# Optimization experiments

Measured on AMD Instinct MI355X. Metric: run time of the kernel, lower is better.

## Reference

```python
import jax, jax.numpy as jnp
import numpy as np

H = 1024
VOCAB = 32000


def setup_inputs() -> dict:
    key = jax.random.key(0)
    ks = jax.random.split(key, 16)
    N, B, T = 32, 64, 400
    s = 1.0 / np.sqrt(H)
    inp = {
        "input_seq": jax.random.randint(ks[0], (N, B), 0, VOCAB),
        "last_hidden": jax.random.normal(ks[1], (1, B, H), jnp.float32),
        "encoder_outputs": jax.random.normal(ks[2], (T, B, H), jnp.float32),
        "encoderB_outputs": jax.random.normal(ks[3], (T, B, H), jnp.float32),
        # parameters
        "emb": jax.random.normal(ks[4], (VOCAB, H), jnp.float32),
        "W_ih": jax.random.uniform(ks[5], (3 * H, H), jnp.float32, -s, s),
        "W_hh": jax.random.uniform(ks[6], (3 * H, H), jnp.float32, -s, s),
        "b_ih": jax.random.uniform(ks[7], (3 * H,), jnp.float32, -s, s),
        "b_hh": jax.random.uniform(ks[8], (3 * H,), jnp.float32, -s, s),
        "attn_W": jax.random.uniform(ks[9], (H, 2 * H), jnp.float32, -s, s),
        "attn_b": jax.random.uniform(ks[10], (H,), jnp.float32, -s, s),
        "attn_v": jax.random.uniform(ks[11], (H,), jnp.float32, -s, s),
        "concat_W": jax.random.uniform(ks[12], (H, 3 * H), jnp.float32, -s, s),
        "concat_b": jax.random.uniform(ks[13], (H,), jnp.float32, -s, s),
        "out_W": jax.random.uniform(ks[14], (VOCAB, H), jnp.float32, -s, s),
        "out_b": jax.random.uniform(ks[15], (VOCAB,), jnp.float32, -s, s),
    }
    return inp


def _gru(x, h0, W_ih, W_hh, b_ih, b_hh):
    # x: (N,B,H), h0: (B,H). PyTorch GRU cell equations.
    def step(h, x_t):
        gi = x_t @ W_ih.T + b_ih          # (B,3H)
        gh = h @ W_hh.T + b_hh
        i_r, i_z, i_n = jnp.split(gi, 3, axis=-1)
        h_r, h_z, h_n = jnp.split(gh, 3, axis=-1)
        r = jax.nn.sigmoid(i_r + h_r)
        z = jax.nn.sigmoid(i_z + h_z)
        n = jnp.tanh(i_n + r * h_n)
        h_new = (1.0 - z) * n + z * h
        return h_new, h_new
    hN, outs = jax.lax.scan(step, h0, x)
    return outs, hN


def _attention(rnn_out, enc, attn_W, attn_b, v):
    # score(h, e) = (Linear([h; e]) ) . v  -- linear in both, so separable.
    W1, W2 = attn_W[:, :H], attn_W[:, H:]
    u1 = W1.T @ v                         # (H,)
    u2 = W2.T @ v
    bias = attn_b @ v                     # scalar
    a = rnn_out @ u1                      # (N,B)
    c = enc @ u2 + bias                   # (T,B)
    # energies (B,N,T), softmax over T (matches F.softmax on (-1, max_len))
    e = a.T[:, :, None] + c.T[:, None, :]
    w = jax.nn.softmax(e, axis=-1)        # (B,N,T)
    ctx = jnp.einsum('bnt,tbh->nbh', w, enc)  # bmm then transpose(0,1)
    return w, ctx


def reference(input_seq, last_hidden, encoder_outputs, encoderB_outputs,
              emb, W_ih, W_hh, b_ih, b_hh, attn_W, attn_b, attn_v,
              concat_W, concat_b, out_W, out_b):
    x = emb[input_seq]                                   # (N,B,H)
    rnn_out, hN = _gru(x, last_hidden[0], W_ih, W_hh, b_ih, b_hh)
    hidden = hN[None]                                    # (1,B,H)
    uw, u_ctx = _attention(rnn_out, encoder_outputs, attn_W, attn_b, attn_v)
    bw, b_ctx = _attention(rnn_out, encoderB_outputs, attn_W, attn_b, attn_v)
    cat = jnp.concatenate([rnn_out, u_ctx, b_ctx], axis=2)   # (N,B,3H)
    h = jnp.tanh(cat @ concat_W.T + concat_b)
    output = h @ out_W.T + out_b                          # (N,B,VOCAB)
    return output, hidden, uw, bw
```

## Files before the change

### kernel.cpp

```cpp
#include <hip/hip_runtime.h>
#include <cstdint>
#include <cstddef>

namespace {

constexpr int kH  = 1024;
constexpr int kB  = 64;
constexpr int kN  = 32;
constexpr int kT  = 400;
constexpr int kV  = 32000;
constexpr int kM  = kN * kB;
constexpr int k3H = 3 * kH;

typedef _Float16 f16;
typedef _Float16 f16x4 __attribute__((ext_vector_type(4)));
typedef _Float16 f16x8 __attribute__((ext_vector_type(8)));
typedef float    f32x4v __attribute__((ext_vector_type(4)));

__device__ __forceinline__ void gload_lds16(const void* g, void* l) {
  __builtin_amdgcn_global_load_lds((__attribute__((address_space(1))) void*)g,
                                   (__attribute__((address_space(3))) void*)l,
                                   16, 0, 0);
}

__device__ __forceinline__ uint32_t pack_f16x2(f16 lo, f16 hi) {
  union { f16 h[2]; uint32_t u; } c;
  c.h[0] = lo; c.h[1] = hi;
  return c.u;
}


__global__ void cvt_f16_kernel(const float* __restrict__ src, f16* __restrict__ dst, int n4) {
  int i = blockIdx.x * blockDim.x + threadIdx.x;
  const int stride = gridDim.x * blockDim.x;
  for (; i < n4; i += stride) {
    float4 v = reinterpret_cast<const float4*>(src)[i];
    f16x4 o = { (f16)v.x, (f16)v.y, (f16)v.z, (f16)v.w };
    reinterpret_cast<f16x4*>(dst)[i] = o;
  }
}

__global__ void gather_x_kernel(const int* __restrict__ seq, const float* __restrict__ emb,
                                f16* __restrict__ xh) {
  const int m = blockIdx.x;
  const int tok = seq[m];
  float4 v = reinterpret_cast<const float4*>(emb + (size_t)tok * kH)[threadIdx.x];
  f16x4 o = { (f16)v.x, (f16)v.y, (f16)v.z, (f16)v.w };
  reinterpret_cast<f16x4*>(xh + (size_t)m * kH)[threadIdx.x] = o;
}

__global__ void init_h_kernel(const float* __restrict__ lh, f16* __restrict__ hh0) {
  const int i = blockIdx.x * blockDim.x + threadIdx.x;
  float4 v = reinterpret_cast<const float4*>(lh)[i];
  f16x4 o = { (f16)v.x, (f16)v.y, (f16)v.z, (f16)v.w };
  reinterpret_cast<f16x4*>(hh0)[i] = o;
}

__global__ void attn_prep_kernel(const float* __restrict__ attn_W, const float* __restrict__ attn_b,
                                 const float* __restrict__ v, float* __restrict__ u2,
                                 float* __restrict__ biasS) {
  const int h = blockIdx.x;
  const int lane = threadIdx.x;
  float sum = 0.0f;
  if (h < kH) {
    for (int k = lane; k < kH; k += 64)
      sum += attn_W[(size_t)k * (2 * kH) + kH + h] * v[k];
  } else {
    for (int k = lane; k < kH; k += 64)
      sum += attn_b[k] * v[k];
  }
  #pragma unroll
  for (int o = 32; o > 0; o >>= 1) sum += __shfl_xor(sum, o);
  if (lane == 0) {
    if (h < kH) u2[h] = sum; else biasS[0] = sum;
  }
}


template <bool TANH, bool NT, typename OUT_T>
__global__ __launch_bounds__(256)
void gemm_bt_kernel(const f16* __restrict__ A, const f16* __restrict__ Bt,
                    const float* __restrict__ bias, OUT_T* __restrict__ C,
                    int M, int N, int K) {
  __shared__ __align__(16) f16 As[128 * 64];
  __shared__ __align__(16) f16 Bs[128 * 64];
  const int tid  = threadIdx.x;
  const int wave = tid >> 6;
  const int lane = tid & 63;
  const int m0 = blockIdx.x * 128;
  const int n0 = blockIdx.y * 128;
  const int wm = (wave >> 1) * 64;
  const int wn = (wave & 1) * 64;
  const int rsub = lane >> 3;
  const int coff = (lane & 7) * 8;
  f32x4v acc[4][4] = {};
  const int nk = K >> 6;
  for (int kc = 0; kc < nk; ++kc) {
    const f16* Ag = A + (size_t)m0 * K + kc * 64;
    const f16* Bg = Bt + (size_t)n0 * K + kc * 64;
    for (int c = wave; c < 16; c += 4) {
      const int row = c * 8 + rsub;
      gload_lds16(Ag + (size_t)row * K + coff, &As[c * 512]);
      gload_lds16(Bg + (size_t)row * K + coff, &Bs[c * 512]);
    }
    __syncthreads();
    #pragma unroll
    for (int kk = 0; kk < 2; ++kk) {
      const int ko = kk * 32 + (lane >> 4) * 8;
      f16x8 af[4], bfr[4];
      #pragma unroll
      for (int i = 0; i < 4; ++i) {
        af[i]  = *reinterpret_cast<const f16x8*>(&As[(wm + i * 16 + (lane & 15)) * 64 + ko]);
        bfr[i] = *reinterpret_cast<const f16x8*>(&Bs[(wn + i * 16 + (lane & 15)) * 64 + ko]);
      }
      #pragma unroll
      for (int mi = 0; mi < 4; ++mi)
        #pragma unroll
        for (int ni = 0; ni < 4; ++ni)
          acc[mi][ni] = __builtin_amdgcn_mfma_f32_16x16x32_f16(af[mi], bfr[ni], acc[mi][ni], 0, 0, 0);
    }
    __syncthreads();
  }
  const int rb = (lane >> 4) * 4;
  const int cb = lane & 15;
  #pragma unroll
  for (int mi = 0; mi < 4; ++mi) {
    #pragma unroll
    for (int ni = 0; ni < 4; ++ni) {
      const int col = n0 + wn + ni * 16 + cb;
      const float bv = bias[col];
      #pragma unroll
      for (int r = 0; r < 4; ++r) {
        const int row = m0 + wm + mi * 16 + rb + r;
        float v = acc[mi][ni][r] + bv;
        if (TANH) v = tanhf(v);
        if (NT) __builtin_nontemporal_store((OUT_T)v, &C[(size_t)row * N + col]);
        else C[(size_t)row * N + col] = (OUT_T)v;
      }
    }
  }
}


constexpr int kGruBlks = 64;
constexpr int kAttnBlks = 128;
constexpr int kCvtBlks = 320;
constexpr int kMegaBlks = kGruBlks + kAttnBlks + kCvtBlks;

__global__ __launch_bounds__(256, 1)
void mega_kernel(const f16* __restrict__ Whh, const float* __restrict__ bhh,
                 const float* __restrict__ gi, const float* __restrict__ lh,
                 f16* __restrict__ HHa, f16* __restrict__ HHb,
                 f16* __restrict__ cath, float* __restrict__ hiddenOut,
                 unsigned int* __restrict__ flags,
                 const float* __restrict__ enc0, const float* __restrict__ enc1,
                 const float* __restrict__ u2, const float* __restrict__ biasS,
                 float* __restrict__ uw, float* __restrict__ bw,
                 const float* __restrict__ oW, f16* __restrict__ oWh,
                 const float* __restrict__ cW, f16* __restrict__ cWh) {
  __shared__ union SM {
    float ghp[4][64][52];
    struct { float4 u2s[256]; float srow[kT]; float red[8]; } at;
  } sm;
  const int bid = blockIdx.x;
  const int tid = threadIdx.x;

  if (bid < kGruBlks) {
    const int wave = tid >> 6;
    const int lane = tid & 63;
    const int ln   = lane & 15;
    const int khi  = lane >> 4;
    const int j0   = bid * 16;
    const int kw   = wave * 256;
    const int fm   = tid >> 2;
    const int fc   = (tid & 3) * 4;
    const int myprod = wave * 16 + ln;

    f16x8 bfr[3][8];
    #pragma unroll
    for (int s = 0; s < 3; ++s)
      #pragma unroll
      for (int ks = 0; ks < 8; ++ks)
        bfr[s][ks] = *reinterpret_cast<const f16x8*>(
            &Whh[(size_t)(s * kH + j0 + ln) * kH + kw + ks * 32 + khi * 8]);

    float hreg[4], bR[4], bZ[4], bN[4];
    #pragma unroll
    for (int e = 0; e < 4; ++e) {
      const int j = j0 + fc + e;
      hreg[e] = lh[(size_t)fm * kH + j];
      bR[e] = bhh[j]; bZ[e] = bhh[kH + j]; bN[e] = bhh[2 * kH + j];
    }

    for (int step = 0; step < kN; ++step) {
      const f16* hh  = (step & 1) ? HHb : HHa;
      f16*       hho = (step & 1) ? HHa : HHb;

      float4 giL[3];
      {
        const size_t mm = (size_t)step * kB + fm;
        #pragma unroll
        for (int s = 0; s < 3; ++s)
          giL[s] = *reinterpret_cast<const float4*>(&gi[mm * k3H + s * kH + j0 + fc]);
      }

      if (step > 0) {
        while (true) {
          unsigned int f = __hip_atomic_load(&flags[myprod], __ATOMIC_RELAXED,
                                             __HIP_MEMORY_SCOPE_SYSTEM);
          if (__all(f >= (unsigned int)step)) break;
          __builtin_amdgcn_s_sleep(1);
        }
        __builtin_amdgcn_fence(__ATOMIC_ACQUIRE, "agent");
      }

      f16x8 af[8][4];
      #pragma unroll
      for (int ks = 0; ks < 8; ++ks)
        #pragma unroll
        for (int mi = 0; mi < 4; ++mi)
          af[ks][mi] = *reinterpret_cast<const f16x8*>(
              &hh[(size_t)(mi * 16 + ln) * kH + kw + ks * 32 + khi * 8]);

      f32x4v acc[4][3] = {};
      #pragma unroll
      for (int ks = 0; ks < 8; ++ks)
        #pragma unroll
        for (int mi = 0; mi < 4; ++mi)
          #pragma unroll
          for (int s = 0; s < 3; ++s)
            acc[mi][s] = __builtin_amdgcn_mfma_f32_16x16x32_f16(af[ks][mi], bfr[s][ks], acc[mi][s], 0, 0, 0);

      #pragma unroll
      for (int mi = 0; mi < 4; ++mi)
        #pragma unroll
        for (int s = 0; s < 3; ++s)
          #pragma unroll
          for (int r = 0; r < 4; ++r)
            sm.ghp[wave][mi * 16 + khi * 4 + r][s * 16 + ln] = acc[mi][s][r];
      __syncthreads();

      float4 gr4 = {0,0,0,0}, gz4 = {0,0,0,0}, gn4 = {0,0,0,0};
      #pragma unroll
      for (int w = 0; w < 4; ++w) {
        float4 a = *reinterpret_cast<const float4*>(&sm.ghp[w][fm][fc]);
        float4 b = *reinterpret_cast<const float4*>(&sm.ghp[w][fm][16 + fc]);
        float4 c = *reinterpret_cast<const float4*>(&sm.ghp[w][fm][32 + fc]);
        gr4.x += a.x; gr4.y += a.y; gr4.z += a.z; gr4.w += a.w;
        gz4.x += b.x; gz4.y += b.y; gz4.z += b.z; gz4.w += b.w;
        gn4.x += c.x; gn4.y += c.y; gn4.z += c.z; gn4.w += c.w;
      }
      float hv[4];
      const float* grp = &gr4.x; const float* gzp = &gz4.x; const float* gnp = &gn4.x;
      const float* gil0 = &giL[0].x; const float* gil1 = &giL[1].x; const float* gil2 = &giL[2].x;
      #pragma unroll
      for (int e = 0; e < 4; ++e) {
        const float r  = 1.0f / (1.0f + expf(-(gil0[e] + grp[e] + bR[e])));
        const float z  = 1.0f / (1.0f + expf(-(gil1[e] + gzp[e] + bZ[e])));
        const float nn = tanhf(gil2[e] + r * (gnp[e] + bN[e]));
        hv[e] = (1.0f - z) * nn + z * hreg[e];
        hreg[e] = hv[e];
      }
      const uint32_t p01 = pack_f16x2((f16)hv[0], (f16)hv[1]);
      const uint32_t p23 = pack_f16x2((f16)hv[2], (f16)hv[3]);
      const unsigned long long pk64 = (unsigned long long)p01 | ((unsigned long long)p23 << 32);
      __hip_atomic_store(reinterpret_cast<unsigned long long*>(&hho[(size_t)fm * kH + j0 + fc]),
                         pk64, __ATOMIC_RELAXED, __HIP_MEMORY_SCOPE_AGENT);
      __syncthreads();
      if (step < kN - 1 && tid == 0)
        __hip_atomic_store(&flags[bid], (unsigned int)(step + 1),
                           __ATOMIC_RELAXED, __HIP_MEMORY_SCOPE_SYSTEM);
      uint2 pku; pku.x = p01; pku.y = p23;
      *reinterpret_cast<uint2*>(&cath[((size_t)step * kB + fm) * k3H + j0 + fc]) = pku;
      if (step == kN - 1) {
        float4 hv4 = { hv[0], hv[1], hv[2], hv[3] };
        *reinterpret_cast<float4*>(&hiddenOut[(size_t)fm * kH + j0 + fc]) = hv4;
      }
    }
  } else if (bid < kGruBlks + kAttnBlks) {
    const int idx = bid - kGruBlks;
    const int e = idx >> 6, b = idx & 63;
    const float* enc = e ? enc1 : enc0;
    const int wave = tid >> 6, lane = tid & 63;

    sm.at.u2s[tid] = *reinterpret_cast<const float4*>(&u2[tid * 4]);
    __syncthreads();
    const float bias = biasS[0];

    for (int t = wave; t < kT; t += 4) {
      const float* row = enc + ((size_t)t * kB + b) * kH + lane * 16;
      float s = 0.0f;
      #pragma unroll
      for (int i = 0; i < 4; ++i) {
        float4 ev = reinterpret_cast<const float4*>(row)[i];
        float4 uv = sm.at.u2s[lane * 4 + i];
        s += ev.x * uv.x + ev.y * uv.y + ev.z * uv.z + ev.w * uv.w;
      }
      #pragma unroll
      for (int o = 32; o > 0; o >>= 1) s += __shfl_xor(s, o);
      if (lane == 0) sm.at.srow[t] = s + bias;
    }
    __syncthreads();

    float lmax = -1e30f;
    for (int t = tid; t < kT; t += 256) lmax = fmaxf(lmax, sm.at.srow[t]);
    #pragma unroll
    for (int o = 32; o > 0; o >>= 1) lmax = fmaxf(lmax, __shfl_xor(lmax, o));
    if (lane == 0) sm.at.red[wave] = lmax;
    __syncthreads();
    const float m = fmaxf(fmaxf(sm.at.red[0], sm.at.red[1]), fmaxf(sm.at.red[2], sm.at.red[3]));
    float lsum = 0.0f;
    for (int t = tid; t < kT; t += 256) {
      float ev = expf(sm.at.srow[t] - m);
      sm.at.srow[t] = ev;
      lsum += ev;
    }
    #pragma unroll
    for (int o = 32; o > 0; o >>= 1) lsum += __shfl_xor(lsum, o);
    if (lane == 0) sm.at.red[4 + wave] = lsum;
    __syncthreads();
    const float inv = 1.0f / (sm.at.red[4] + sm.at.red[5] + sm.at.red[6] + sm.at.red[7]);
    for (int t = tid; t < kT; t += 256) sm.at.srow[t] *= inv;
    __syncthreads();

    float* outp = (e ? bw : uw) + (size_t)b * kN * kT;
    for (int n = 0; n < kN; ++n)
      for (int t = tid; t < kT; t += 256)
        __builtin_nontemporal_store(sm.at.srow[t], &outp[n * kT + t]);

    const int j = tid * 4;
    float4 acc = {0,0,0,0};
    for (int t = 0; t < kT; ++t) {
      const float wt = sm.at.srow[t];
      const float4 ev = *reinterpret_cast<const float4*>(&enc[((size_t)t * kB + b) * kH + j]);
      acc.x += wt * ev.x; acc.y += wt * ev.y; acc.z += wt * ev.z; acc.w += wt * ev.w;
    }
    f16x4 cv = { (f16)acc.x, (f16)acc.y, (f16)acc.z, (f16)acc.w };
    #pragma unroll
    for (int n = 0; n < kN; ++n)
      *reinterpret_cast<f16x4*>(&cath[((size_t)(n * kB + b)) * k3H + kH + e * kH + j]) = cv;
  } else {
    constexpr int nOW = kV * kH / 4;
    constexpr int nCW = kH * k3H / 4;
    const int stride = kCvtBlks * 256;
    for (int i = (bid - kGruBlks - kAttnBlks) * 256 + tid; i < nOW + nCW; i += stride) {
      if (i < nOW) {
        float4 v = reinterpret_cast<const float4*>(oW)[i];
        f16x4 o = { (f16)v.x, (f16)v.y, (f16)v.z, (f16)v.w };
        reinterpret_cast<f16x4*>(oWh)[i] = o;
      } else {
        const int k = i - nOW;
        float4 v = reinterpret_cast<const float4*>(cW)[k];
        f16x4 o = { (f16)v.x, (f16)v.y, (f16)v.z, (f16)v.w };
        reinterpret_cast<f16x4*>(cWh)[k] = o;
      }
    }
  }
}

}


extern "C" void kernel_launch(void* const* d_in, const int* in_sizes, int n_in,
                              void* d_out, int out_size, void* d_ws, size_t ws_size,
                              hipStream_t stream) {
  (void)in_sizes; (void)n_in; (void)out_size; (void)ws_size;
  const int*   seq    = (const int*)d_in[0];
  const float* lh     = (const float*)d_in[1];
  const float* enc0   = (const float*)d_in[2];
  const float* enc1   = (const float*)d_in[3];
  const float* emb    = (const float*)d_in[4];
  const float* W_ih   = (const float*)d_in[5];
  const float* W_hh   = (const float*)d_in[6];
  const float* b_ih   = (const float*)d_in[7];
  const float* b_hh   = (const float*)d_in[8];
  const float* attn_W = (const float*)d_in[9];
  const float* attn_b = (const float*)d_in[10];
  const float* attn_v = (const float*)d_in[11];
  const float* cW     = (const float*)d_in[12];
  const float* cb     = (const float*)d_in[13];
  const float* oW     = (const float*)d_in[14];
  const float* ob     = (const float*)d_in[15];
  float* out = (float*)d_out;

  char* ws = (char*)d_ws;
  constexpr size_t oWih = 0;
  constexpr size_t oWhh = oWih + 6291456;
  constexpr size_t oCW  = oWhh + 6291456;
  constexpr size_t oOW  = oCW + 6291456;
  constexpr size_t oX   = oOW + 65536000;
  constexpr size_t oGI  = oX + 4194304;
  constexpr size_t oH0  = oGI + 25165824;
  constexpr size_t oH1  = oH0 + 262144;
  constexpr size_t oHH0 = oH1 + 262144;
  constexpr size_t oHH1 = oHH0 + 131072;
  constexpr size_t oCAT = oHH1 + 131072;
  constexpr size_t oH2  = oCAT + 12582912;
  constexpr size_t oU2  = oH2 + 4194304;
  constexpr size_t oBS  = oU2 + 4096;
  constexpr size_t oC   = oBS + 256;
  constexpr size_t oWSM = oC + 204800;
  constexpr size_t oCTR = oWSM + 204800;

  f16*   Wih_h = (f16*)(ws + oWih);
  f16*   Whh_h = (f16*)(ws + oWhh);
  f16*   cW_h  = (f16*)(ws + oCW);
  f16*   oW_h  = (f16*)(ws + oOW);
  f16*   X_h   = (f16*)(ws + oX);
  float* GI    = (float*)(ws + oGI);
  f16*   HH0   = (f16*)(ws + oHH0);
  f16*   HH1   = (f16*)(ws + oHH1);
  f16*   CAT   = (f16*)(ws + oCAT);
  f16*   H2    = (f16*)(ws + oH2);
  float* U2    = (float*)(ws + oU2);
  float* BS    = (float*)(ws + oBS);
  unsigned int* FLAGS = (unsigned int*)(ws + oCTR);

  constexpr size_t oHidden = (size_t)kM * kV;
  constexpr size_t oUW = oHidden + (size_t)kB * kH;
  constexpr size_t oBW = oUW + (size_t)kB * kN * kT;

  cvt_f16_kernel<<<1024, 256, 0, stream>>>(W_ih, Wih_h, k3H * kH / 4);
  cvt_f16_kernel<<<1024, 256, 0, stream>>>(W_hh, Whh_h, k3H * kH / 4);
  gather_x_kernel<<<kM, 256, 0, stream>>>(seq, emb, X_h);
  init_h_kernel<<<64, 256, 0, stream>>>(lh, HH0);
  attn_prep_kernel<<<1025, 64, 0, stream>>>(attn_W, attn_b, attn_v, U2, BS);
  hipMemsetAsync(FLAGS, 0, 64 * sizeof(unsigned int), stream);

  gemm_bt_kernel<false, false, float><<<dim3(16, 24), 256, 0, stream>>>(X_h, Wih_h, b_ih, GI, kM, k3H, kH);

  mega_kernel<<<kMegaBlks, 256, 0, stream>>>(Whh_h, b_hh, GI, lh, HH0, HH1, CAT,
                                             out + oHidden, FLAGS,
                                             enc0, enc1, U2, BS,
                                             out + oUW, out + oBW,
                                             oW, oW_h, cW, cW_h);

  gemm_bt_kernel<true, false, f16><<<dim3(16, 8), 256, 0, stream>>>(CAT, cW_h, cb, H2, kM, kH, k3H);
  gemm_bt_kernel<false, true, float><<<dim3(16, 250), 256, 0, stream>>>(H2, oW_h, ob, out, kM, kV, kH);
}
```

Baseline: 691.4 us.

## Fuse prep kernels, stage GEMM epilogues through LDS, remap output GEMM blocks

Merges the weight conversion, embedding gather, hidden-state init and attention prep kernels into one launch to cut launch overhead. GEMM epilogues now stage results through shared memory so stores go out as full-row vectors instead of scattered scalar writes. The large vocab GEMM gets a 1D grid with an XCD-aware block remap meant to improve L2 reuse of the A matrix. The costs are extra syncs and LDS traffic in the epilogue, plus an LDS union that changes the shared-memory footprint.

```diff
diff --git a/kernel.cpp b/kernel.cpp
--- a/kernel.cpp
+++ b/kernel.cpp
@@ -30,65 +30,83 @@
 }
 
 
-__global__ void cvt_f16_kernel(const float* __restrict__ src, f16* __restrict__ dst, int n4) {
-  int i = blockIdx.x * blockDim.x + threadIdx.x;
-  const int stride = gridDim.x * blockDim.x;
-  for (; i < n4; i += stride) {
-    float4 v = reinterpret_cast<const float4*>(src)[i];
-    f16x4 o = { (f16)v.x, (f16)v.y, (f16)v.z, (f16)v.w };
-    reinterpret_cast<f16x4*>(dst)[i] = o;
+__global__ __launch_bounds__(256)
+void pre_kernel(const float* __restrict__ Wih, f16* __restrict__ WihH,
+                const float* __restrict__ Whh, f16* __restrict__ WhhH,
+                const int* __restrict__ seq, const float* __restrict__ emb,
+                f16* __restrict__ Xh, const float* __restrict__ lh,
+                f16* __restrict__ HH0,
+                const float* __restrict__ attnW, const float* __restrict__ attnB,
+                const float* __restrict__ attnV,
+                float* __restrict__ u2, float* __restrict__ biasS) {
+  const int bid = blockIdx.x, tid = threadIdx.x;
+  if (bid < 512) {
+    const float* src = (bid < 256) ? Wih : Whh;
+    f16* dst = (bid < 256) ? WihH : WhhH;
+    constexpr int n4 = k3H * kH / 4;
+    for (int i = (bid & 255) * 256 + tid; i < n4; i += 256 * 256) {
+      float4 v = reinterpret_cast<const float4*>(src)[i];
+      f16x4 o = { (f16)v.x, (f16)v.y, (f16)v.z, (f16)v.w };
+      reinterpret_cast<f16x4*>(dst)[i] = o;
+    }
+  } else if (bid < 640) {
+    const int m0 = (bid - 512) * 16;
+    for (int k = 0; k < 16; ++k) {
+      const int m = m0 + k;
+      const int tok = seq[m];
+      float4 v = reinterpret_cast<const float4*>(emb + (size_t)tok * kH)[tid];
+      f16x4 o = { (f16)v.x, (f16)v.y, (f16)v.z, (f16)v.w };
+      reinterpret_cast<f16x4*>(Xh + (size_t)m * kH)[tid] = o;
+    }
+  } else if (bid < 644) {
+    for (int i = (bid - 640) * 256 + tid; i < 16384; i += 1024) {
+      float4 v = reinterpret_cast<const float4*>(lh)[i];
+      f16x4 o = { (f16)v.x, (f16)v.y, (f16)v.z, (f16)v.w };
+      reinterpret_cast<f16x4*>(HH0)[i] = o;
+    }
+  } else {
+    const int item = (bid - 644) * 4 + (tid >> 6);
+    const int lane = tid & 63;
+    if (item > kH) return;
+    float sum = 0.0f;
+    if (item < kH) {
+      for (int k = lane; k < kH; k += 64)
+        sum += attnW[(size_t)k * (2 * kH) + kH + item] * attnV[k];
+    } else {
+      for (int k = lane; k < kH; k += 64)
+        sum += attnB[k] * attnV[k];
+    }
+    #pragma unroll
+    for (int o = 32; o > 0; o >>= 1) sum += __shfl_xor(sum, o);
+    if (lane == 0) { if (item < kH) u2[item] = sum; else biasS[0] = sum; }
   }
 }
 
-__global__ void gather_x_kernel(const int* __restrict__ seq, const float* __restrict__ emb,
-                                f16* __restrict__ xh) {
-  const int m = blockIdx.x;
-  const int tok = seq[m];
-  float4 v = reinterpret_cast<const float4*>(emb + (size_t)tok * kH)[threadIdx.x];
-  f16x4 o = { (f16)v.x, (f16)v.y, (f16)v.z, (f16)v.w };
-  reinterpret_cast<f16x4*>(xh + (size_t)m * kH)[threadIdx.x] = o;
-}
-
-__global__ void init_h_kernel(const float* __restrict__ lh, f16* __restrict__ hh0) {
-  const int i = blockIdx.x * blockDim.x + threadIdx.x;
-  float4 v = reinterpret_cast<const float4*>(lh)[i];
-  f16x4 o = { (f16)v.x, (f16)v.y, (f16)v.z, (f16)v.w };
-  reinterpret_cast<f16x4*>(hh0)[i] = o;
-}
-
-__global__ void attn_prep_kernel(const float* __restrict__ attn_W, const float* __restrict__ attn_b,
-                                 const float* __restrict__ v, float* __restrict__ u2,
-                                 float* __restrict__ biasS) {
-  const int h = blockIdx.x;
-  const int lane = threadIdx.x;
-  float sum = 0.0f;
-  if (h < kH) {
-    for (int k = lane; k < kH; k += 64)
-      sum += attn_W[(size_t)k * (2 * kH) + kH + h] * v[k];
+
+template <int MODE, typename OUT_T>
+__global__ __launch_bounds__(256)
+void gemm_bt2_kernel(const f16* __restrict__ A, const f16* __restrict__ Bt,
+                     const float* __restrict__ bias, OUT_T* __restrict__ C,
+                     int M, int N, int K) {
+  __shared__ union {
+    struct { __align__(16) f16 As[128 * 64]; __align__(16) f16 Bs[128 * 64]; } st;
+    float rp32[64][132];
+    f16   rp16[128][132];
+  } sm;
+  int bx, by;
+  if (MODE == 2) {
+    const int nrow = M >> 7;
+    const int cpx  = gridDim.x >> 3;
+    const int wgid = (blockIdx.x & 7) * cpx + (blockIdx.x >> 3);
+    bx = wgid % nrow;  by = wgid / nrow;
   } else {
-    for (int k = lane; k < kH; k += 64)
-      sum += attn_b[k] * v[k];
+    bx = blockIdx.x;  by = blockIdx.y;
   }
-  #pragma unroll
-  for (int o = 32; o > 0; o >>= 1) sum += __shfl_xor(sum, o);
-  if (lane == 0) {
-    if (h < kH) u2[h] = sum; else biasS[0] = sum;
-  }
-}
-
-
-template <bool TANH, bool NT, typename OUT_T>
-__global__ __launch_bounds__(256)
-void gemm_bt_kernel(const f16* __restrict__ A, const f16* __restrict__ Bt,
-                    const float* __restrict__ bias, OUT_T* __restrict__ C,
-                    int M, int N, int K) {
-  __shared__ __align__(16) f16 As[128 * 64];
-  __shared__ __align__(16) f16 Bs[128 * 64];
   const int tid  = threadIdx.x;
   const int wave = tid >> 6;
   const int lane = tid & 63;
-  const int m0 = blockIdx.x * 128;
-  const int n0 = blockIdx.y * 128;
+  const int m0 = bx * 128;
+  const int n0 = by * 128;
   const int wm = (wave >> 1) * 64;
   const int wn = (wave & 1) * 64;
   const int rsub = lane >> 3;
@@ -100,8 +118,8 @@
     const f16* Bg = Bt + (size_t)n0 * K + kc * 64;
     for (int c = wave; c < 16; c += 4) {
       const int row = c * 8 + rsub;
-      gload_lds16(Ag + (size_t)row * K + coff, &As[c * 512]);
-      gload_lds16(Bg + (size_t)row * K + coff, &Bs[c * 512]);
+      gload_lds16(Ag + (size_t)row * K + coff, &sm.st.As[c * 512]);
+      gload_lds16(Bg + (size_t)row * K + coff, &sm.st.Bs[c * 512]);
     }
     __syncthreads();
     #pragma unroll
@@ -110,8 +128,8 @@
       f16x8 af[4], bfr[4];
       #pragma unroll
       for (int i = 0; i < 4; ++i) {
-        af[i]  = *reinterpret_cast<const f16x8*>(&As[(wm + i * 16 + (lane & 15)) * 64 + ko]);
-        bfr[i] = *reinterpret_cast<const f16x8*>(&Bs[(wn + i * 16 + (lane & 15)) * 64 + ko]);
+        af[i]  = *reinterpret_cast<const f16x8*>(&sm.st.As[(wm + i * 16 + (lane & 15)) * 64 + ko]);
+        bfr[i] = *reinterpret_cast<const f16x8*>(&sm.st.Bs[(wn + i * 16 + (lane & 15)) * 64 + ko]);
       }
       #pragma unroll
       for (int mi = 0; mi < 4; ++mi)
@@ -123,19 +141,53 @@
   }
   const int rb = (lane >> 4) * 4;
   const int cb = lane & 15;
-  #pragma unroll
-  for (int mi = 0; mi < 4; ++mi) {
-    #pragma unroll
-    for (int ni = 0; ni < 4; ++ni) {
-      const int col = n0 + wn + ni * 16 + cb;
-      const float bv = bias[col];
-      #pragma unroll
-      for (int r = 0; r < 4; ++r) {
-        const int row = m0 + wm + mi * 16 + rb + r;
-        float v = acc[mi][ni][r] + bv;
-        if (TANH) v = tanhf(v);
-        if (NT) __builtin_nontemporal_store((OUT_T)v, &C[(size_t)row * N + col]);
-        else C[(size_t)row * N + col] = (OUT_T)v;
+
+  if (MODE == 1) {
+    #pragma unroll
+    for (int mi = 0; mi < 4; ++mi)
+      #pragma unroll
+      for (int ni = 0; ni < 4; ++ni) {
+        const int col = wn + ni * 16 + cb;
+        const float bv = bias[n0 + col];
+        #pragma unroll
+        for (int r = 0; r < 4; ++r)
+          sm.rp16[wm + mi * 16 + rb + r][col] = (f16)tanhf(acc[mi][ni][r] + bv);
+      }
+    __syncthreads();
+    #pragma unroll
+    for (int i = 0; i < 8; ++i) {
+      const int idx = i * 256 + tid;
+      const int row = idx >> 4;
+      const int c8  = (idx & 15) * 8;
+      f16x8 v = *reinterpret_cast<const f16x8*>(&sm.rp16[row][c8]);
+      *reinterpret_cast<f16x8*>(&C[(size_t)(m0 + row) * N + n0 + c8]) = v;
+    }
+  } else {
+    #pragma unroll
+    for (int half = 0; half < 2; ++half) {
+      __syncthreads();
+      if ((wm >> 6) == half) {
+        #pragma unroll
+        for (int mi = 0; mi < 4; ++mi)
+          #pragma unroll
+          for (int ni = 0; ni < 4; ++ni) {
+            const int col = wn + ni * 16 + cb;
+            const float bv = bias[n0 + col];
+            #pragma unroll
+            for (int r = 0; r < 4; ++r)
+              sm.rp32[mi * 16 + rb + r][col] = acc[mi][ni][r] + bv;
+          }
+      }
+      __syncthreads();
+      #pragma unroll
+      for (int i = 0; i < 8; ++i) {
+        const int idx = i * 256 + tid;
+        const int row = idx >> 5;
+        const int c4  = (idx & 31) * 4;
+        f32x4v v = *reinterpret_cast<const f32x4v*>(&sm.rp32[row][c4]);
+        float* dst = (float*)&C[(size_t)(m0 + half * 64 + row) * N + n0 + c4];
+        if (MODE == 2) __builtin_nontemporal_store(v, reinterpret_cast<f32x4v*>(dst));
+        else *reinterpret_cast<f32x4v*>(dst) = v;
       }
     }
   }
@@ -164,10 +216,10 @@
   } sm;
   const int bid = blockIdx.x;
   const int tid = threadIdx.x;
+  const int wave = tid >> 6;
+  const int lane = tid & 63;
 
   if (bid < kGruBlks) {
-    const int wave = tid >> 6;
-    const int lane = tid & 63;
     const int ln   = lane & 15;
     const int khi  = lane >> 4;
     const int j0   = bid * 16;
@@ -252,12 +304,12 @@
       }
       float hv[4];
       const float* grp = &gr4.x; const float* gzp = &gz4.x; const float* gnp = &gn4.x;
-      const float* gil0 = &giL[0].x; const float* gil1 = &giL[1].x; const float* gil2 = &giL[2].x;
+      const float* g0 = &giL[0].x; const float* g1 = &giL[1].x; const float* g2 = &giL[2].x;
       #pragma unroll
       for (int e = 0; e < 4; ++e) {
-        const float r  = 1.0f / (1.0f + expf(-(gil0[e] + grp[e] + bR[e])));
-        const float z  = 1.0f / (1.0f + expf(-(gil1[e] + gzp[e] + bZ[e])));
-        const float nn = tanhf(gil2[e] + r * (gnp[e] + bN[e]));
+        const float r  = 1.0f / (1.0f + expf(-(g0[e] + grp[e] + bR[e])));
+        const float z  = 1.0f / (1.0f + expf(-(g1[e] + gzp[e] + bZ[e])));
+        const float nn = tanhf(g2[e] + r * (gnp[e] + bN[e]));
         hv[e] = (1.0f - z) * nn + z * hreg[e];
         hreg[e] = hv[e];
       }
@@ -281,7 +333,6 @@
     const int idx = bid - kGruBlks;
     const int e = idx >> 6, b = idx & 63;
     const float* enc = e ? enc1 : enc0;
-    const int wave = tid >> 6, lane = tid & 63;
 
     sm.at.u2s[tid] = *reinterpret_cast<const float4*>(&u2[tid * 4]);
     __syncthreads();
@@ -390,17 +441,13 @@
   constexpr size_t oOW  = oCW + 6291456;
   constexpr size_t oX   = oOW + 65536000;
   constexpr size_t oGI  = oX + 4194304;
-  constexpr size_t oH0  = oGI + 25165824;
-  constexpr size_t oH1  = oH0 + 262144;
-  constexpr size_t oHH0 = oH1 + 262144;
+  constexpr size_t oHH0 = oGI + 25165824;
   constexpr size_t oHH1 = oHH0 + 131072;
   constexpr size_t oCAT = oHH1 + 131072;
   constexpr size_t oH2  = oCAT + 12582912;
   constexpr size_t oU2  = oH2 + 4194304;
   constexpr size_t oBS  = oU2 + 4096;
-  constexpr size_t oC   = oBS + 256;
-  constexpr size_t oWSM = oC + 204800;
-  constexpr size_t oCTR = oWSM + 204800;
+  constexpr size_t oCTR = oBS + 256;
 
   f16*   Wih_h = (f16*)(ws + oWih);
   f16*   Whh_h = (f16*)(ws + oWhh);
@@ -420,14 +467,11 @@
   constexpr size_t oUW = oHidden + (size_t)kB * kH;
   constexpr size_t oBW = oUW + (size_t)kB * kN * kT;
 
-  cvt_f16_kernel<<<1024, 256, 0, stream>>>(W_ih, Wih_h, k3H * kH / 4);
-  cvt_f16_kernel<<<1024, 256, 0, stream>>>(W_hh, Whh_h, k3H * kH / 4);
-  gather_x_kernel<<<kM, 256, 0, stream>>>(seq, emb, X_h);
-  init_h_kernel<<<64, 256, 0, stream>>>(lh, HH0);
-  attn_prep_kernel<<<1025, 64, 0, stream>>>(attn_W, attn_b, attn_v, U2, BS);
-  hipMemsetAsync(FLAGS, 0, 64 * sizeof(unsigned int), stream);
-
-  gemm_bt_kernel<false, false, float><<<dim3(16, 24), 256, 0, stream>>>(X_h, Wih_h, b_ih, GI, kM, k3H, kH);
+  pre_kernel<<<901, 256, 0, stream>>>(W_ih, Wih_h, W_hh, Whh_h, seq, emb, X_h,
+                                      lh, HH0, attn_W, attn_b, attn_v, U2, BS);
+  (void)hipMemsetAsync(FLAGS, 0, 64 * sizeof(unsigned int), stream);
+
+  gemm_bt2_kernel<0, float><<<dim3(16, 24), 256, 0, stream>>>(X_h, Wih_h, b_ih, GI, kM, k3H, kH);
 
   mega_kernel<<<kMegaBlks, 256, 0, stream>>>(Whh_h, b_hh, GI, lh, HH0, HH1, CAT,
                                              out + oHidden, FLAGS,
@@ -435,6 +479,6 @@
                                              out + oUW, out + oBW,
                                              oW, oW_h, cW, cW_h);
 
-  gemm_bt_kernel<true, false, f16><<<dim3(16, 8), 256, 0, stream>>>(CAT, cW_h, cb, H2, kM, kH, k3H);
-  gemm_bt_kernel<false, true, float><<<dim3(16, 250), 256, 0, stream>>>(H2, oW_h, ob, out, kM, kV, kH);
-}
+  gemm_bt2_kernel<1, f16><<<dim3(16, 8), 256, 0, stream>>>(CAT, cW_h, cb, H2, kM, kH, k3H);
+  gemm_bt2_kernel<2, float><<<4000, 256, 0, stream>>>(H2, oW_h, ob, out, kM, kV, kH);
+}
```

After: 715.6 us. 1.04x slower.
